# Performance work log

Measured on AMD Instinct MI355X. Metric: run time of the kernel, lower is better.

## Reference

```python
import jax, jax.numpy as jnp
import numpy as np

N = 50000
E_RAND = 800000
IN_CH = 128
HID = 128
HEADS = 8
HEAD_DIM = HID // HEADS  # 16
NUM_CLASSES = 40
NEG_SLOPE = 0.2


def _gatv2_conv(x, src, dst, Wl, Wr, att, b, concat):
    # Wl, Wr: [F_in, H*C]; att: [H, C]; b: [H*C] or [C]
    H, C = att.shape
    xl = (x @ Wl).reshape(N, H, C)  # source-side projection
    xr = (x @ Wr).reshape(N, H, C)  # target-side projection
    e = jax.nn.leaky_relu(xl[src] + xr[dst], NEG_SLOPE)      # [E,H,C]
    logits = jnp.einsum('ehc,hc->eh', e, att)                # [E,H]
    lmax = jax.ops.segment_max(logits, dst, num_segments=N)  # [N,H]
    lmax = jnp.where(jnp.isfinite(lmax), lmax, 0.0)
    p = jnp.exp(logits - lmax[dst])                          # [E,H]
    denom = jax.ops.segment_sum(p, dst, num_segments=N)      # [N,H]
    alpha = p / jnp.maximum(denom[dst], 1e-16)               # segment softmax
    out = jax.ops.segment_sum(xl[src] * alpha[:, :, None], dst, num_segments=N)  # [N,H,C]
    out = out.reshape(N, H * C) if concat else out.mean(axis=1)
    return out + b


def setup_inputs() -> dict:
    key = jax.random.key(0)
    ks = jax.random.split(key, 16)
    x = jax.random.normal(ks[0], (N, IN_CH), dtype=jnp.float32)
    src = jax.random.randint(ks[1], (E_RAND,), 0, N)
    dst = jax.random.randint(ks[2], (E_RAND,), 0, N)
    loops = jnp.arange(N)  # PyG GATv2Conv adds self-loops by default
    edge_src = jnp.concatenate([src, loops]).astype(jnp.int64)
    edge_dst = jnp.concatenate([dst, loops]).astype(jnp.int64)

    def glorot(k, shape):
        fan = shape[0] + shape[1]
        s = jnp.sqrt(6.0 / fan)
        return jax.random.uniform(k, shape, jnp.float32, -s, s)

    # layer 0: 128 -> 8 heads x 16, concat
    Wl0 = glorot(ks[3], (IN_CH, HID)); Wr0 = glorot(ks[4], (IN_CH, HID))
    att0 = glorot(ks[5], (HEADS, HEAD_DIM)); b0 = jnp.zeros((HID,), jnp.float32)
    # layer 1: 128 -> 8 heads x 16, concat
    Wl1 = glorot(ks[6], (HID, HID)); Wr1 = glorot(ks[7], (HID, HID))
    att1 = glorot(ks[8], (HEADS, HEAD_DIM)); b1 = jnp.zeros((HID,), jnp.float32)
    # layer 2: 128 -> 1 head x 40, no concat (mean == identity for 1 head)
    Wl2 = glorot(ks[9], (HID, NUM_CLASSES)); Wr2 = glorot(ks[10], (HID, NUM_CLASSES))
    att2 = glorot(ks[11], (1, NUM_CLASSES)); b2 = jnp.zeros((NUM_CLASSES,), jnp.float32)

    return {"x": x, "edge_src": edge_src, "edge_dst": edge_dst,
            "Wl0": Wl0, "Wr0": Wr0, "att0": att0, "b0": b0,
            "Wl1": Wl1, "Wr1": Wr1, "att1": att1, "b1": b1,
            "Wl2": Wl2, "Wr2": Wr2, "att2": att2, "b2": b2}


def reference(x, edge_src, edge_dst, Wl0, Wr0, att0, b0, Wl1, Wr1, att1, b1,
              Wl2, Wr2, att2, b2):
    # Inference mode: F.dropout(training=False) is identity.
    h = _gatv2_conv(x, edge_src, edge_dst, Wl0, Wr0, att0, b0, concat=True)
    h = jax.nn.relu(h)
    h = _gatv2_conv(h, edge_src, edge_dst, Wl1, Wr1, att1, b1, concat=True)
    h = jax.nn.relu(h)
    out = _gatv2_conv(h, edge_src, edge_dst, Wl2, Wr2, att2, b2, concat=False)
    return out
```

## Files before the change

kernel.cpp:

```cpp
#include <hip/hip_runtime.h>
#include <hip/hip_fp16.h>
#include <cmath>

typedef _Float16 half8 __attribute__((ext_vector_type(8)));
typedef _Float16 h2 __attribute__((ext_vector_type(2)));
typedef float f32x4 __attribute__((ext_vector_type(4)));

#define BINCAP 2600
#define BSTRIDE (BINCAP + 384)
#define NBINS_MAX 512

__global__ void fill_i32(int* __restrict__ p, int v, int n) {
    int i = blockIdx.x * blockDim.x + threadIdx.x;
    if (i < n) p[i] = v;
}

__device__ __forceinline__ float dpp_add_xor1(float t) {
    int r = __builtin_amdgcn_update_dpp(0, __float_as_int(t), 0xB1, 0xF, 0xF, true);
    return t + __int_as_float(r);
}
__device__ __forceinline__ float dpp_add_xor2(float t) {
    int r = __builtin_amdgcn_update_dpp(0, __float_as_int(t), 0x4E, 0xF, 0xF, true);
    return t + __int_as_float(r);
}

__device__ __forceinline__ float hdot2(h2 a, h2 b, float acc) {
#if __has_builtin(__builtin_amdgcn_fdot2)
    return __builtin_amdgcn_fdot2(a, b, acc, false);
#else
    return acc + (float)a[0] * (float)b[0] + (float)a[1] * (float)b[1];
#endif
}

__global__ __launch_bounds__(256) void bin_edges(const int* __restrict__ src,
                                                 const int* __restrict__ dst,
                                                 int* __restrict__ binCnt,
                                                 unsigned* __restrict__ binned,
                                                 int E, int nbins)
{
    __shared__ int hist[NBINS_MAX];
    __shared__ int ofs[NBINS_MAX];
    int tid = threadIdx.x;
    for (int i = tid; i < nbins; i += 256) hist[i] = 0;
    __syncthreads();
    int chunk = (E + gridDim.x - 1) / gridDim.x;
    int e0 = blockIdx.x * chunk;
    int e1 = min(e0 + chunk, E);
    for (int e = e0 + tid; e < e1; e += 256)
        atomicAdd(&hist[dst[e] >> 7], 1);
    __syncthreads();
    for (int b = tid; b < nbins; b += 256) {
        int h = hist[b];
        ofs[b] = (h > 0) ? atomicAdd(&binCnt[b], h) : 0;
    }
    __syncthreads();
    for (int e = e0 + tid; e < e1; e += 256) {
        int d = dst[e];
        int b = d >> 7;
        int p = atomicAdd(&ofs[b], 1);
        if (p < BINCAP)
            binned[(size_t)b * BINCAP + p] = (unsigned)src[e] | ((unsigned)(d & 127) << 16);
    }
}

__global__ __launch_bounds__(256) void bin_to_csr(const int* __restrict__ binCnt,
                                                  const unsigned* __restrict__ binned,
                                                  int* __restrict__ bucket,
                                                  int2* __restrict__ meta, int N)
{
    __shared__ int dcnt[128], ps[128], dpos[128];
    __shared__ int sbuf[BSTRIDE];
    __shared__ int tot_s;
    int b = blockIdx.x, tid = threadIdx.x;
    int nb = min(binCnt[b], BINCAP);
    size_t inbase = (size_t)b * BINCAP;
    size_t outbase = (size_t)b * BSTRIDE;
    if (tid < 128) dcnt[tid] = 0;
    __syncthreads();
    for (int i = tid; i < nb; i += 256)
        atomicAdd(&dcnt[(binned[inbase + i] >> 16) & 127], 1);
    __syncthreads();
    int pc = 0;
    if (tid < 128) { pc = (dcnt[tid] + 3) & ~3; ps[tid] = pc; }
    __syncthreads();
    for (int o = 1; o < 128; o <<= 1) {
        int v = (tid < 128 && tid >= o) ? ps[tid - o] : 0;
        __syncthreads();
        if (tid < 128) ps[tid] += v;
        __syncthreads();
    }
    if (tid < 128) {
        int dofs = ps[tid] - pc;
        dpos[tid] = dofs;
        for (int k = dcnt[tid]; k < pc; ++k) sbuf[dofs + k] = 0;
        int gd = b * 128 + tid;
        if (gd < N) meta[gd] = make_int2((int)outbase + dofs, dcnt[tid]);
        if (tid == 127) tot_s = ps[127];
    }
    __syncthreads();
    for (int i = tid; i < nb; i += 256) {
        unsigned u = binned[inbase + i];
        int p = atomicAdd(&dpos[(u >> 16) & 127], 1);
        sbuf[p] = (int)(u & 0xFFFFu);
    }
    __syncthreads();
    int tot = min(tot_s, BSTRIDE);
    for (int i = tid; i < tot; i += 256)
        bucket[outbase + i] = sbuf[i];
}

__global__ void wt_build(const float* __restrict__ Wl0, const float* __restrict__ Wr0,
                         const float* __restrict__ Wl1, const float* __restrict__ Wr1,
                         const float* __restrict__ Wl2, const float* __restrict__ Wr2,
                         __half* __restrict__ Wt0, __half* __restrict__ Wt1,
                         __half* __restrict__ Wt2) {
    int i = blockIdx.x * blockDim.x + threadIdx.x;
    const int T01 = 256 * 128, T2 = 80 * 128;
    if (i < T01) {
        int c = i >> 7, k = i & 127;
        float v = (c < 128) ? Wl0[k * 128 + c] : Wr0[k * 128 + (c - 128)];
        Wt0[i] = __float2half(v);
    } else if (i < 2 * T01) {
        int j = i - T01;
        int c = j >> 7, k = j & 127;
        float v = (c < 128) ? Wl1[k * 128 + c] : Wr1[k * 128 + (c - 128)];
        Wt1[j] = __float2half(v);
    } else if (i < 2 * T01 + T2) {
        int j = i - 2 * T01;
        int c = j >> 7, k = j & 127;
        float v = (c < 40) ? Wl2[k * 40 + c] : Wr2[k * 40 + (c - 40)];
        Wt2[j] = __float2half(v);
    }
}

template<int OUTH, bool HIN>
__global__ __launch_bounds__(256) void proj_mfma(const void* __restrict__ xin,
                                                 const __half* __restrict__ Wt,
                                                 __half* __restrict__ xl,
                                                 __half* __restrict__ xr,
                                                 int n)
{
    constexpr int OUTT = 2 * OUTH;
    constexpr int CT = OUTT / 16;
    __shared__ uint4 lds[1024 + OUTT * 16];
    int t = threadIdx.x;
    int r0 = blockIdx.x * 64;
    {
        int row = t >> 2;
        int k0 = (t & 3) * 32;
        int gr = r0 + row;
        #pragma unroll
        for (int s = 0; s < 4; ++s) {
            union { uint4 u; _Float16 h[8]; } pk;
            if (gr < n) {
                if constexpr (HIN) {
                    const uint4* xp = (const uint4*)((const __half*)xin + (size_t)gr * 128 + k0);
                    pk.u = xp[s];
                } else {
                    const float4* xp = (const float4*)((const float*)xin + (size_t)gr * 128 + k0 + s * 8);
                    float4 f0 = xp[0], f1 = xp[1];
                    pk.h[0] = (_Float16)f0.x; pk.h[1] = (_Float16)f0.y;
                    pk.h[2] = (_Float16)f0.z; pk.h[3] = (_Float16)f0.w;
                    pk.h[4] = (_Float16)f1.x; pk.h[5] = (_Float16)f1.y;
                    pk.h[6] = (_Float16)f1.z; pk.h[7] = (_Float16)f1.w;
                }
            } else {
                pk.u = make_uint4(0, 0, 0, 0);
            }
            int j = (t & 3) * 4 + s;
            lds[row * 16 + (j ^ (row & 7))] = pk.u;
        }
    }
    {
        const uint4* Wtv = (const uint4*)Wt;
        for (int m = t; m < OUTT * 16; m += 256) {
            int c = m >> 4, j = m & 15;
            lds[1024 + c * 16 + (j ^ (c & 7))] = Wtv[m];
        }
    }
    __syncthreads();
    int w = t >> 6, l = t & 63;
    int lr = l & 15, lg = l >> 4;
    half8 af[4];
    {
        int row = w * 16 + lr;
        #pragma unroll
        for (int kb = 0; kb < 4; ++kb) {
            int j = kb * 4 + lg;
            af[kb] = *reinterpret_cast<const half8*>(&lds[row * 16 + (j ^ (row & 7))]);
        }
    }
    f32x4 acc[CT];
    #pragma unroll
    for (int ct = 0; ct < CT; ++ct) acc[ct] = (f32x4){0.f, 0.f, 0.f, 0.f};
    int csw = lr & 7;
    #pragma unroll
    for (int ct = 0; ct < CT; ++ct) {
        int c = ct * 16 + lr;
        #pragma unroll
        for (int kb = 0; kb < 4; ++kb) {
            int j = kb * 4 + lg;
            half8 bf = *reinterpret_cast<const half8*>(&lds[1024 + c * 16 + (j ^ csw)]);
            acc[ct] = __builtin_amdgcn_mfma_f32_16x16x32_f16(af[kb], bf, acc[ct], 0, 0, 0);
        }
    }
    #pragma unroll
    for (int ct = 0; ct < CT; ++ct) {
        int c = ct * 16 + lr;
        #pragma unroll
        for (int i = 0; i < 4; ++i) {
            int gr = r0 + w * 16 + lg * 4 + i;
            if (gr < n) {
                __half h = __float2half(acc[ct][i]);
                if (c < OUTH) xl[(size_t)gr * OUTH + c] = h;
                else          xr[(size_t)gr * OUTH + (c - OUTH)] = h;
            }
        }
    }
}

__global__ void aggr128(const int2* __restrict__ meta, const int* __restrict__ bucket,
                        const __half* __restrict__ xlh, const __half* __restrict__ xrh,
                        const float* __restrict__ att, const float* __restrict__ bias,
                        __half* __restrict__ outp, int N, int do_relu)
{
    int wave = threadIdx.x >> 6;
    int lane = threadIdx.x & 63;
    int grp = lane >> 4;
    int j = lane & 15;
    int nd = (blockIdx.x * (blockDim.x >> 6) + wave) * 4 + grp;
    if (nd >= N) return;
    union { uint4 u; h2 h[4]; } rq;
    rq.u = ((const uint4*)xrh)[(size_t)nd * 16 + j];
    h2 a2[4];
    {
        float4 t0 = ((const float4*)att)[2 * j];
        float4 t1 = ((const float4*)att)[2 * j + 1];
        a2[0] = h2{(_Float16)t0.x, (_Float16)t0.y};
        a2[1] = h2{(_Float16)t0.z, (_Float16)t0.w};
        a2[2] = h2{(_Float16)t1.x, (_Float16)t1.y};
        a2[3] = h2{(_Float16)t1.z, (_Float16)t1.w};
    }
    const uint4* xlv = (const uint4*)xlh;
    int2 md = meta[nd];
    int beg = md.x, deg = md.y;
    const int* brow = bucket + beg;
    const h2 c02 = h2{(_Float16)0.2f, (_Float16)0.2f};
    float s0 = 0.f, s1 = 0.f, s2 = 0.f, s3 = 0.f;
    float o0[8], o1[8], o2[8], o3[8];
    #pragma unroll
    for (int i = 0; i < 8; ++i) { o0[i] = 0.f; o1[i] = 0.f; o2[i] = 0.f; o3[i] = 0.f; }
    for (int p = 0; p < deg; p += 4) {
        int4 ss = *(const int4*)(brow + p);
        union { uint4 u; h2 h[4]; } q0, q1, q2, q3;
        q0.u = xlv[(size_t)ss.x * 16 + j];
        q1.u = xlv[(size_t)ss.y * 16 + j];
        q2.u = xlv[(size_t)ss.z * 16 + j];
        q3.u = xlv[(size_t)ss.w * 16 + j];
        {
            float t = 0.f;
            #pragma unroll
            for (int i = 0; i < 4; ++i) {
                h2 v2 = q0.h[i] + rq.h[i];
                h2 lk = __builtin_elementwise_max(v2, v2 * c02);
                t = hdot2(lk, a2[i], t);
            }
            t = dpp_add_xor1(t);
            float pe = __expf(t);
            s0 += pe;
            #pragma unroll
            for (int i = 0; i < 4; ++i) {
                o0[2*i]   = fmaf(pe, (float)q0.h[i][0], o0[2*i]);
                o0[2*i+1] = fmaf(pe, (float)q0.h[i][1], o0[2*i+1]);
            }
        }
        {
            float t = 0.f;
            #pragma unroll
            for (int i = 0; i < 4; ++i) {
                h2 v2 = q1.h[i] + rq.h[i];
                h2 lk = __builtin_elementwise_max(v2, v2 * c02);
                t = hdot2(lk, a2[i], t);
            }
            t = dpp_add_xor1(t);
            float pe = (p + 1 < deg) ? __expf(t) : 0.f;
            s1 += pe;
            #pragma unroll
            for (int i = 0; i < 4; ++i) {
                o1[2*i]   = fmaf(pe, (float)q1.h[i][0], o1[2*i]);
                o1[2*i+1] = fmaf(pe, (float)q1.h[i][1], o1[2*i+1]);
            }
        }
        {
            float t = 0.f;
            #pragma unroll
            for (int i = 0; i < 4; ++i) {
                h2 v2 = q2.h[i] + rq.h[i];
                h2 lk = __builtin_elementwise_max(v2, v2 * c02);
                t = hdot2(lk, a2[i], t);
            }
            t = dpp_add_xor1(t);
            float pe = (p + 2 < deg) ? __expf(t) : 0.f;
            s2 += pe;
            #pragma unroll
            for (int i = 0; i < 4; ++i) {
                o2[2*i]   = fmaf(pe, (float)q2.h[i][0], o2[2*i]);
                o2[2*i+1] = fmaf(pe, (float)q2.h[i][1], o2[2*i+1]);
            }
        }
        {
            float t = 0.f;
            #pragma unroll
            for (int i = 0; i < 4; ++i) {
                h2 v2 = q3.h[i] + rq.h[i];
                h2 lk = __builtin_elementwise_max(v2, v2 * c02);
                t = hdot2(lk, a2[i], t);
            }
            t = dpp_add_xor1(t);
            float pe = (p + 3 < deg) ? __expf(t) : 0.f;
            s3 += pe;
            #pragma unroll
            for (int i = 0; i < 4; ++i) {
                o3[2*i]   = fmaf(pe, (float)q3.h[i][0], o3[2*i]);
                o3[2*i+1] = fmaf(pe, (float)q3.h[i][1], o3[2*i+1]);
            }
        }
    }
    float s = (s0 + s1) + (s2 + s3);
    {
        float inv = 1.f / fmaxf(s, 1e-16f);
        float4 b0 = ((const float4*)bias)[2 * j];
        float4 b1 = ((const float4*)bias)[2 * j + 1];
        float w[8];
        #pragma unroll
        for (int i = 0; i < 8; ++i)
            w[i] = ((o0[i] + o1[i]) + (o2[i] + o3[i])) * inv;
        w[0] += b0.x; w[1] += b0.y; w[2] += b0.z; w[3] += b0.w;
        w[4] += b1.x; w[5] += b1.y; w[6] += b1.z; w[7] += b1.w;
        if (do_relu) {
            #pragma unroll
            for (int i = 0; i < 8; ++i) w[i] = fmaxf(w[i], 0.f);
        }
        union { uint4 u; __half2 h[4]; } ow;
        ow.h[0] = __floats2half2_rn(w[0], w[1]);
        ow.h[1] = __floats2half2_rn(w[2], w[3]);
        ow.h[2] = __floats2half2_rn(w[4], w[5]);
        ow.h[3] = __floats2half2_rn(w[6], w[7]);
        ((uint4*)outp)[(size_t)nd * 16 + j] = ow.u;
    }
}

__global__ void aggr40(const int2* __restrict__ meta, const int* __restrict__ bucket,
                       const __half* __restrict__ xlh, const __half* __restrict__ xrh,
                       const float* __restrict__ att, const float* __restrict__ bias,
                       float* __restrict__ outp, int N)
{
    int wave = threadIdx.x >> 6;
    int lane = threadIdx.x & 63;
    int grp = lane >> 4;
    int j = lane & 15;
    int nd = (blockIdx.x * (blockDim.x >> 6) + wave) * 4 + grp;
    if (nd >= N) return;
    bool act = (j < 10);
    union { uint2 u; h2 h[2]; } rq;
    rq.u = make_uint2(0, 0);
    h2 a2[2] = {h2{(_Float16)0.f, (_Float16)0.f}, h2{(_Float16)0.f, (_Float16)0.f}};
    if (act) {
        rq.u = *(const uint2*)(xrh + (size_t)nd * 40 + 4 * j);
        float4 a4 = ((const float4*)att)[j];
        a2[0] = h2{(_Float16)a4.x, (_Float16)a4.y};
        a2[1] = h2{(_Float16)a4.z, (_Float16)a4.w};
    }
    int2 md = meta[nd];
    int beg = md.x, deg = md.y;
    const int* brow = bucket + beg;
    const h2 c02 = h2{(_Float16)0.2f, (_Float16)0.2f};
    float s0 = 0.f, s1 = 0.f;
    float o0[4], o1[4];
    #pragma unroll
    for (int i = 0; i < 4; ++i) { o0[i] = 0.f; o1[i] = 0.f; }
    for (int p = 0; p < deg; p += 4) {
        int4 ss = *(const int4*)(brow + p);
        union { uint2 u; h2 h[2]; } q0, q1, q2, q3;
        q0.u = act ? *(const uint2*)(xlh + (size_t)ss.x * 40 + 4 * j) : make_uint2(0, 0);
        q1.u = act ? *(const uint2*)(xlh + (size_t)ss.y * 40 + 4 * j) : make_uint2(0, 0);
        q2.u = act ? *(const uint2*)(xlh + (size_t)ss.z * 40 + 4 * j) : make_uint2(0, 0);
        q3.u = act ? *(const uint2*)(xlh + (size_t)ss.w * 40 + 4 * j) : make_uint2(0, 0);
        {
            float t = 0.f;
            #pragma unroll
            for (int i = 0; i < 2; ++i) {
                h2 v2 = q0.h[i] + rq.h[i];
                h2 lk = __builtin_elementwise_max(v2, v2 * c02);
                t = hdot2(lk, a2[i], t);
            }
            t = dpp_add_xor1(t); t = dpp_add_xor2(t);
            t += __shfl_xor(t, 4); t += __shfl_xor(t, 8);
            float pe = __expf(t);
            s0 += pe;
            #pragma unroll
            for (int i = 0; i < 2; ++i) {
                o0[2*i]   = fmaf(pe, (float)q0.h[i][0], o0[2*i]);
                o0[2*i+1] = fmaf(pe, (float)q0.h[i][1], o0[2*i+1]);
            }
        }
        {
            float t = 0.f;
            #pragma unroll
            for (int i = 0; i < 2; ++i) {
                h2 v2 = q1.h[i] + rq.h[i];
                h2 lk = __builtin_elementwise_max(v2, v2 * c02);
                t = hdot2(lk, a2[i], t);
            }
            t = dpp_add_xor1(t); t = dpp_add_xor2(t);
            t += __shfl_xor(t, 4); t += __shfl_xor(t, 8);
            float pe = (p + 1 < deg) ? __expf(t) : 0.f;
            s1 += pe;
            #pragma unroll
            for (int i = 0; i < 2; ++i) {
                o1[2*i]   = fmaf(pe, (float)q1.h[i][0], o1[2*i]);
                o1[2*i+1] = fmaf(pe, (float)q1.h[i][1], o1[2*i+1]);
            }
        }
        {
            float t = 0.f;
            #pragma unroll
            for (int i = 0; i < 2; ++i) {
                h2 v2 = q2.h[i] + rq.h[i];
                h2 lk = __builtin_elementwise_max(v2, v2 * c02);
                t = hdot2(lk, a2[i], t);
            }
            t = dpp_add_xor1(t); t = dpp_add_xor2(t);
            t += __shfl_xor(t, 4); t += __shfl_xor(t, 8);
            float pe = (p + 2 < deg) ? __expf(t) : 0.f;
            s0 += pe;
            #pragma unroll
            for (int i = 0; i < 2; ++i) {
                o0[2*i]   = fmaf(pe, (float)q2.h[i][0], o0[2*i]);
                o0[2*i+1] = fmaf(pe, (float)q2.h[i][1], o0[2*i+1]);
            }
        }
        {
            float t = 0.f;
            #pragma unroll
            for (int i = 0; i < 2; ++i) {
                h2 v2 = q3.h[i] + rq.h[i];
                h2 lk = __builtin_elementwise_max(v2, v2 * c02);
                t = hdot2(lk, a2[i], t);
            }
            t = dpp_add_xor1(t); t = dpp_add_xor2(t);
            t += __shfl_xor(t, 4); t += __shfl_xor(t, 8);
            float pe = (p + 3 < deg) ? __expf(t) : 0.f;
            s1 += pe;
            #pragma unroll
            for (int i = 0; i < 2; ++i) {
                o1[2*i]   = fmaf(pe, (float)q3.h[i][0], o1[2*i]);
                o1[2*i+1] = fmaf(pe, (float)q3.h[i][1], o1[2*i+1]);
            }
        }
    }
    if (act) {
        float s = s0 + s1;
        float inv = 1.f / fmaxf(s, 1e-16f);
        float4 b4 = ((const float4*)bias)[j];
        float4 w;
        w.x = (o0[0] + o1[0]) * inv + b4.x;
        w.y = (o0[1] + o1[1]) * inv + b4.y;
        w.z = (o0[2] + o1[2]) * inv + b4.z;
        w.w = (o0[3] + o1[3]) * inv + b4.w;
        *(float4*)(outp + (size_t)nd * 40 + 4 * j) = w;
    }
}

extern "C" void kernel_launch(void* const* d_in, const int* in_sizes, int n_in,
                              void* d_out, int out_size, void* d_ws, size_t ws_size,
                              hipStream_t stream)
{
    const float* x    = (const float*)d_in[0];
    const int*   esrc = (const int*)d_in[1];
    const int*   edst = (const int*)d_in[2];
    const float* Wl0  = (const float*)d_in[3];
    const float* Wr0  = (const float*)d_in[4];
    const float* att0 = (const float*)d_in[5];
    const float* b0   = (const float*)d_in[6];
    const float* Wl1  = (const float*)d_in[7];
    const float* Wr1  = (const float*)d_in[8];
    const float* att1 = (const float*)d_in[9];
    const float* b1   = (const float*)d_in[10];
    const float* Wl2  = (const float*)d_in[11];
    const float* Wr2  = (const float*)d_in[12];
    const float* att2 = (const float*)d_in[13];
    const float* b2   = (const float*)d_in[14];
    float* out = (float*)d_out;

    const int N = in_sizes[0] / 128;
    const int E = in_sizes[1];
    const int nbins = (N + 127) / 128;

    char* ws = (char*)d_ws;
    size_t off = 0;
    auto walloc = [&](size_t bytes) -> void* {
        void* p = ws + off;
        off = (off + bytes + 255) & ~(size_t)255;
        return p;
    };
    __half*   xlh    = (__half*)walloc((size_t)N * 128 * 2);
    __half*   xrh    = (__half*)walloc((size_t)N * 128 * 2);
    __half*   hbuf   = (__half*)walloc((size_t)N * 128 * 2);
    __half*   Wt0    = (__half*)walloc(256 * 128 * 2);
    __half*   Wt1    = (__half*)walloc(256 * 128 * 2);
    __half*   Wt2    = (__half*)walloc(80 * 128 * 2);
    int*      binCnt = (int*)walloc((size_t)nbins * 4);
    unsigned* binned = (unsigned*)walloc((size_t)nbins * BINCAP * 4);
    int*      bucket = (int*)walloc((size_t)nbins * BSTRIDE * 4);
    int2*     meta   = (int2*)walloc((size_t)N * 8);

    wt_build<<<(2 * 256 * 128 + 80 * 128 + 255) / 256, 256, 0, stream>>>(
        Wl0, Wr0, Wl1, Wr1, Wl2, Wr2, Wt0, Wt1, Wt2);

    fill_i32<<<(nbins + 255) / 256, 256, 0, stream>>>(binCnt, 0, nbins);
    bin_edges<<<256, 256, 0, stream>>>(esrc, edst, binCnt, binned, E, nbins);
    bin_to_csr<<<nbins, 256, 0, stream>>>(binCnt, binned, bucket, meta, N);

    int nblk = (N + 15) / 16;
    int pblk = (N + 63) / 64;

    proj_mfma<128, false><<<pblk, 256, 0, stream>>>(x, Wt0, xlh, xrh, N);
    aggr128<<<nblk, 256, 0, stream>>>(meta, bucket, xlh, xrh, att0, b0, hbuf, N, 1);
    proj_mfma<128, true><<<pblk, 256, 0, stream>>>(hbuf, Wt1, xlh, xrh, N);
    aggr128<<<nblk, 256, 0, stream>>>(meta, bucket, xlh, xrh, att1, b1, hbuf, N, 1);
    proj_mfma<40, true><<<pblk, 256, 0, stream>>>(hbuf, Wt2, xlh, xrh, N);
    aggr40<<<nblk, 256, 0, stream>>>(meta, bucket, xlh, xrh, att2, b2, out, N);
}
```

Baseline: 180.7 us.

## Sort destination nodes by degree and software-pipeline neighbor gathers in aggregation

Adds a degree histogram, scan and scatter that build a permutation of nodes grouped by in-degree, so each wave's four node groups get similar edge counts and idle less on divergent loop trip counts. The aggregation kernels also prefetch the next four neighbor rows while computing the current four, to hide gather latency. The fill kernel is replaced by hipMemsetAsync. This adds three small kernels plus extra live registers for the prefetch buffers, and output writes follow the permuted node order.

```diff
diff --git a/kernel.cpp b/kernel.cpp
--- a/kernel.cpp
+++ b/kernel.cpp
@@ -9,11 +9,6 @@
 #define BINCAP 2600
 #define BSTRIDE (BINCAP + 384)
 #define NBINS_MAX 512
-
-__global__ void fill_i32(int* __restrict__ p, int v, int n) {
-    int i = blockIdx.x * blockDim.x + threadIdx.x;
-    if (i < n) p[i] = v;
-}
 
 __device__ __forceinline__ float dpp_add_xor1(float t) {
     int r = __builtin_amdgcn_update_dpp(0, __float_as_int(t), 0xB1, 0xF, 0xF, true);
@@ -107,6 +102,44 @@
     int tot = min(tot_s, BSTRIDE);
     for (int i = tid; i < tot; i += 256)
         bucket[outbase + i] = sbuf[i];
+}
+
+__global__ void deg_hist(const int2* __restrict__ meta, int* __restrict__ hist, int N) {
+    __shared__ int lh[256];
+    int tid = threadIdx.x;
+    lh[tid] = 0;
+    __syncthreads();
+    int i = blockIdx.x * blockDim.x + tid;
+    int stride = gridDim.x * blockDim.x;
+    for (; i < N; i += stride)
+        atomicAdd(&lh[min(meta[i].y, 255)], 1);
+    __syncthreads();
+    if (lh[tid] > 0) atomicAdd(&hist[tid], lh[tid]);
+}
+
+__global__ void scan_hist(const int* __restrict__ hist, int* __restrict__ dofs) {
+    __shared__ int b[256];
+    int t = threadIdx.x;
+    int v = hist[t];
+    b[t] = v;
+    __syncthreads();
+    for (int o = 1; o < 256; o <<= 1) {
+        int x = (t >= o) ? b[t - o] : 0;
+        __syncthreads();
+        b[t] += x;
+        __syncthreads();
+    }
+    dofs[t] = b[t] - v;
+}
+
+__global__ void perm_scatter(const int2* __restrict__ meta, int* __restrict__ dofs,
+                             int* __restrict__ perm, int N) {
+    int i = blockIdx.x * blockDim.x + threadIdx.x;
+    int stride = gridDim.x * blockDim.x;
+    for (; i < N; i += stride) {
+        int pos = atomicAdd(&dofs[min(meta[i].y, 255)], 1);
+        perm[pos] = i;
+    }
 }
 
 __global__ void wt_build(const float* __restrict__ Wl0, const float* __restrict__ Wr0,
@@ -219,7 +252,8 @@
     }
 }
 
-__global__ void aggr128(const int2* __restrict__ meta, const int* __restrict__ bucket,
+__global__ void aggr128(const int* __restrict__ perm,
+                        const int2* __restrict__ meta, const int* __restrict__ bucket,
                         const __half* __restrict__ xlh, const __half* __restrict__ xrh,
                         const float* __restrict__ att, const float* __restrict__ bias,
                         __half* __restrict__ outp, int N, int do_relu)
@@ -228,8 +262,9 @@
     int lane = threadIdx.x & 63;
     int grp = lane >> 4;
     int j = lane & 15;
-    int nd = (blockIdx.x * (blockDim.x >> 6) + wave) * 4 + grp;
-    if (nd >= N) return;
+    int ndv = (blockIdx.x * (blockDim.x >> 6) + wave) * 4 + grp;
+    if (ndv >= N) return;
+    int nd = perm[ndv];
     union { uint4 u; h2 h[4]; } rq;
     rq.u = ((const uint4*)xrh)[(size_t)nd * 16 + j];
     h2 a2[4];
@@ -250,18 +285,31 @@
     float o0[8], o1[8], o2[8], o3[8];
     #pragma unroll
     for (int i = 0; i < 8; ++i) { o0[i] = 0.f; o1[i] = 0.f; o2[i] = 0.f; o3[i] = 0.f; }
+    uint4 qa0, qa1, qa2, qa3;
+    {
+        int4 ss = *(const int4*)(brow);
+        qa0 = xlv[(size_t)ss.x * 16 + j];
+        qa1 = xlv[(size_t)ss.y * 16 + j];
+        qa2 = xlv[(size_t)ss.z * 16 + j];
+        qa3 = xlv[(size_t)ss.w * 16 + j];
+    }
     for (int p = 0; p < deg; p += 4) {
-        int4 ss = *(const int4*)(brow + p);
-        union { uint4 u; h2 h[4]; } q0, q1, q2, q3;
-        q0.u = xlv[(size_t)ss.x * 16 + j];
-        q1.u = xlv[(size_t)ss.y * 16 + j];
-        q2.u = xlv[(size_t)ss.z * 16 + j];
-        q3.u = xlv[(size_t)ss.w * 16 + j];
-        {
-            float t = 0.f;
-            #pragma unroll
-            for (int i = 0; i < 4; ++i) {
-                h2 v2 = q0.h[i] + rq.h[i];
+        uint4 qb0, qb1, qb2, qb3;
+        {
+            int pn = (p + 4 < deg) ? p + 4 : p;
+            int4 sn = *(const int4*)(brow + pn);
+            qb0 = xlv[(size_t)sn.x * 16 + j];
+            qb1 = xlv[(size_t)sn.y * 16 + j];
+            qb2 = xlv[(size_t)sn.z * 16 + j];
+            qb3 = xlv[(size_t)sn.w * 16 + j];
+        }
+        union { uint4 u; h2 h[4]; } q;
+        {
+            q.u = qa0;
+            float t = 0.f;
+            #pragma unroll
+            for (int i = 0; i < 4; ++i) {
+                h2 v2 = q.h[i] + rq.h[i];
                 h2 lk = __builtin_elementwise_max(v2, v2 * c02);
                 t = hdot2(lk, a2[i], t);
             }
@@ -270,15 +318,16 @@
             s0 += pe;
             #pragma unroll
             for (int i = 0; i < 4; ++i) {
-                o0[2*i]   = fmaf(pe, (float)q0.h[i][0], o0[2*i]);
-                o0[2*i+1] = fmaf(pe, (float)q0.h[i][1], o0[2*i+1]);
-            }
-        }
-        {
-            float t = 0.f;
-            #pragma unroll
-            for (int i = 0; i < 4; ++i) {
-                h2 v2 = q1.h[i] + rq.h[i];
+                o0[2*i]   = fmaf(pe, (float)q.h[i][0], o0[2*i]);
+                o0[2*i+1] = fmaf(pe, (float)q.h[i][1], o0[2*i+1]);
+            }
+        }
+        {
+            q.u = qa1;
+            float t = 0.f;
+            #pragma unroll
+            for (int i = 0; i < 4; ++i) {
+                h2 v2 = q.h[i] + rq.h[i];
                 h2 lk = __builtin_elementwise_max(v2, v2 * c02);
                 t = hdot2(lk, a2[i], t);
             }
@@ -287,15 +336,16 @@
             s1 += pe;
             #pragma unroll
             for (int i = 0; i < 4; ++i) {
-                o1[2*i]   = fmaf(pe, (float)q1.h[i][0], o1[2*i]);
-                o1[2*i+1] = fmaf(pe, (float)q1.h[i][1], o1[2*i+1]);
-            }
-        }
-        {
-            float t = 0.f;
-            #pragma unroll
-            for (int i = 0; i < 4; ++i) {
-                h2 v2 = q2.h[i] + rq.h[i];
+                o1[2*i]   = fmaf(pe, (float)q.h[i][0], o1[2*i]);
+                o1[2*i+1] = fmaf(pe, (float)q.h[i][1], o1[2*i+1]);
+            }
+        }
+        {
+            q.u = qa2;
+            float t = 0.f;
+            #pragma unroll
+            for (int i = 0; i < 4; ++i) {
+                h2 v2 = q.h[i] + rq.h[i];
                 h2 lk = __builtin_elementwise_max(v2, v2 * c02);
                 t = hdot2(lk, a2[i], t);
             }
@@ -304,15 +354,16 @@
             s2 += pe;
             #pragma unroll
             for (int i = 0; i < 4; ++i) {
-                o2[2*i]   = fmaf(pe, (float)q2.h[i][0], o2[2*i]);
-                o2[2*i+1] = fmaf(pe, (float)q2.h[i][1], o2[2*i+1]);
-            }
-        }
-        {
-            float t = 0.f;
-            #pragma unroll
-            for (int i = 0; i < 4; ++i) {
-                h2 v2 = q3.h[i] + rq.h[i];
+                o2[2*i]   = fmaf(pe, (float)q.h[i][0], o2[2*i]);
+                o2[2*i+1] = fmaf(pe, (float)q.h[i][1], o2[2*i+1]);
+            }
+        }
+        {
+            q.u = qa3;
+            float t = 0.f;
+            #pragma unroll
+            for (int i = 0; i < 4; ++i) {
+                h2 v2 = q.h[i] + rq.h[i];
                 h2 lk = __builtin_elementwise_max(v2, v2 * c02);
                 t = hdot2(lk, a2[i], t);
             }
@@ -321,10 +372,11 @@
             s3 += pe;
             #pragma unroll
             for (int i = 0; i < 4; ++i) {
-                o3[2*i]   = fmaf(pe, (float)q3.h[i][0], o3[2*i]);
-                o3[2*i+1] = fmaf(pe, (float)q3.h[i][1], o3[2*i+1]);
-            }
-        }
+                o3[2*i]   = fmaf(pe, (float)q.h[i][0], o3[2*i]);
+                o3[2*i+1] = fmaf(pe, (float)q.h[i][1], o3[2*i+1]);
+            }
+        }
+        qa0 = qb0; qa1 = qb1; qa2 = qb2; qa3 = qb3;
     }
     float s = (s0 + s1) + (s2 + s3);
     {
@@ -350,7 +402,8 @@
     }
 }
 
-__global__ void aggr40(const int2* __restrict__ meta, const int* __restrict__ bucket,
+__global__ void aggr40(const int* __restrict__ perm,
+                       const int2* __restrict__ meta, const int* __restrict__ bucket,
                        const __half* __restrict__ xlh, const __half* __restrict__ xrh,
                        const float* __restrict__ att, const float* __restrict__ bias,
                        float* __restrict__ outp, int N)
@@ -359,8 +412,9 @@
     int lane = threadIdx.x & 63;
     int grp = lane >> 4;
     int j = lane & 15;
-    int nd = (blockIdx.x * (blockDim.x >> 6) + wave) * 4 + grp;
-    if (nd >= N) return;
+    int ndv = (blockIdx.x * (blockDim.x >> 6) + wave) * 4 + grp;
+    if (ndv >= N) return;
+    int nd = perm[ndv];
     bool act = (j < 10);
     union { uint2 u; h2 h[2]; } rq;
     rq.u = make_uint2(0, 0);
@@ -379,18 +433,31 @@
     float o0[4], o1[4];
     #pragma unroll
     for (int i = 0; i < 4; ++i) { o0[i] = 0.f; o1[i] = 0.f; }
+    uint2 qa0, qa1, qa2, qa3;
+    {
+        int4 ss = *(const int4*)(brow);
+        qa0 = act ? *(const uint2*)(xlh + (size_t)ss.x * 40 + 4 * j) : make_uint2(0, 0);
+        qa1 = act ? *(const uint2*)(xlh + (size_t)ss.y * 40 + 4 * j) : make_uint2(0, 0);
+        qa2 = act ? *(const uint2*)(xlh + (size_t)ss.z * 40 + 4 * j) : make_uint2(0, 0);
+        qa3 = act ? *(const uint2*)(xlh + (size_t)ss.w * 40 + 4 * j) : make_uint2(0, 0);
+    }
     for (int p = 0; p < deg; p += 4) {
-        int4 ss = *(const int4*)(brow + p);
-        union { uint2 u; h2 h[2]; } q0, q1, q2, q3;
-        q0.u = act ? *(const uint2*)(xlh + (size_t)ss.x * 40 + 4 * j) : make_uint2(0, 0);
-        q1.u = act ? *(const uint2*)(xlh + (size_t)ss.y * 40 + 4 * j) : make_uint2(0, 0);
-        q2.u = act ? *(const uint2*)(xlh + (size_t)ss.z * 40 + 4 * j) : make_uint2(0, 0);
-        q3.u = act ? *(const uint2*)(xlh + (size_t)ss.w * 40 + 4 * j) : make_uint2(0, 0);
-        {
-            float t = 0.f;
-            #pragma unroll
-            for (int i = 0; i < 2; ++i) {
-                h2 v2 = q0.h[i] + rq.h[i];
+        uint2 qb0, qb1, qb2, qb3;
+        {
+            int pn = (p + 4 < deg) ? p + 4 : p;
+            int4 sn = *(const int4*)(brow + pn);
+            qb0 = act ? *(const uint2*)(xlh + (size_t)sn.x * 40 + 4 * j) : make_uint2(0, 0);
+            qb1 = act ? *(const uint2*)(xlh + (size_t)sn.y * 40 + 4 * j) : make_uint2(0, 0);
+            qb2 = act ? *(const uint2*)(xlh + (size_t)sn.z * 40 + 4 * j) : make_uint2(0, 0);
+            qb3 = act ? *(const uint2*)(xlh + (size_t)sn.w * 40 + 4 * j) : make_uint2(0, 0);
+        }
+        union { uint2 u; h2 h[2]; } q;
+        {
+            q.u = qa0;
+            float t = 0.f;
+            #pragma unroll
+            for (int i = 0; i < 2; ++i) {
+                h2 v2 = q.h[i] + rq.h[i];
                 h2 lk = __builtin_elementwise_max(v2, v2 * c02);
                 t = hdot2(lk, a2[i], t);
             }
@@ -400,15 +467,16 @@
             s0 += pe;
             #pragma unroll
             for (int i = 0; i < 2; ++i) {
-                o0[2*i]   = fmaf(pe, (float)q0.h[i][0], o0[2*i]);
-                o0[2*i+1] = fmaf(pe, (float)q0.h[i][1], o0[2*i+1]);
-            }
-        }
-        {
-            float t = 0.f;
-            #pragma unroll
-            for (int i = 0; i < 2; ++i) {
-                h2 v2 = q1.h[i] + rq.h[i];
+                o0[2*i]   = fmaf(pe, (float)q.h[i][0], o0[2*i]);
+                o0[2*i+1] = fmaf(pe, (float)q.h[i][1], o0[2*i+1]);
+            }
+        }
+        {
+            q.u = qa1;
+            float t = 0.f;
+            #pragma unroll
+            for (int i = 0; i < 2; ++i) {
+                h2 v2 = q.h[i] + rq.h[i];
                 h2 lk = __builtin_elementwise_max(v2, v2 * c02);
                 t = hdot2(lk, a2[i], t);
             }
@@ -418,15 +486,16 @@
             s1 += pe;
             #pragma unroll
             for (int i = 0; i < 2; ++i) {
-                o1[2*i]   = fmaf(pe, (float)q1.h[i][0], o1[2*i]);
-                o1[2*i+1] = fmaf(pe, (float)q1.h[i][1], o1[2*i+1]);
-            }
-        }
-        {
-            float t = 0.f;
-            #pragma unroll
-            for (int i = 0; i < 2; ++i) {
-                h2 v2 = q2.h[i] + rq.h[i];
+                o1[2*i]   = fmaf(pe, (float)q.h[i][0], o1[2*i]);
+                o1[2*i+1] = fmaf(pe, (float)q.h[i][1], o1[2*i+1]);
+            }
+        }
+        {
+            q.u = qa2;
+            float t = 0.f;
+            #pragma unroll
+            for (int i = 0; i < 2; ++i) {
+                h2 v2 = q.h[i] + rq.h[i];
                 h2 lk = __builtin_elementwise_max(v2, v2 * c02);
                 t = hdot2(lk, a2[i], t);
             }
@@ -436,15 +505,16 @@
             s0 += pe;
             #pragma unroll
             for (int i = 0; i < 2; ++i) {
-                o0[2*i]   = fmaf(pe, (float)q2.h[i][0], o0[2*i]);
-                o0[2*i+1] = fmaf(pe, (float)q2.h[i][1], o0[2*i+1]);
-            }
-        }
-        {
-            float t = 0.f;
-            #pragma unroll
-            for (int i = 0; i < 2; ++i) {
-                h2 v2 = q3.h[i] + rq.h[i];
+                o0[2*i]   = fmaf(pe, (float)q.h[i][0], o0[2*i]);
+                o0[2*i+1] = fmaf(pe, (float)q.h[i][1], o0[2*i+1]);
+            }
+        }
+        {
+            q.u = qa3;
+            float t = 0.f;
+            #pragma unroll
+            for (int i = 0; i < 2; ++i) {
+                h2 v2 = q.h[i] + rq.h[i];
                 h2 lk = __builtin_elementwise_max(v2, v2 * c02);
                 t = hdot2(lk, a2[i], t);
             }
@@ -454,10 +524,11 @@
             s1 += pe;
             #pragma unroll
             for (int i = 0; i < 2; ++i) {
-                o1[2*i]   = fmaf(pe, (float)q3.h[i][0], o1[2*i]);
-                o1[2*i+1] = fmaf(pe, (float)q3.h[i][1], o1[2*i+1]);
-            }
-        }
+                o1[2*i]   = fmaf(pe, (float)q.h[i][0], o1[2*i]);
+                o1[2*i+1] = fmaf(pe, (float)q.h[i][1], o1[2*i+1]);
+            }
+        }
+        qa0 = qb0; qa1 = qb1; qa2 = qb2; qa3 = qb3;
     }
     if (act) {
         float s = s0 + s1;
@@ -514,21 +585,29 @@
     unsigned* binned = (unsigned*)walloc((size_t)nbins * BINCAP * 4);
     int*      bucket = (int*)walloc((size_t)nbins * BSTRIDE * 4);
     int2*     meta   = (int2*)walloc((size_t)N * 8);
+    int*      hist   = (int*)walloc(256 * 4);
+    int*      dofs   = (int*)walloc(256 * 4);
+    int*      perm   = (int*)walloc((size_t)N * 4);
 
     wt_build<<<(2 * 256 * 128 + 80 * 128 + 255) / 256, 256, 0, stream>>>(
         Wl0, Wr0, Wl1, Wr1, Wl2, Wr2, Wt0, Wt1, Wt2);
 
-    fill_i32<<<(nbins + 255) / 256, 256, 0, stream>>>(binCnt, 0, nbins);
+    hipMemsetAsync(binCnt, 0, (size_t)nbins * 4, stream);
+    hipMemsetAsync(hist, 0, 256 * 4, stream);
     bin_edges<<<256, 256, 0, stream>>>(esrc, edst, binCnt, binned, E, nbins);
     bin_to_csr<<<nbins, 256, 0, stream>>>(binCnt, binned, bucket, meta, N);
 
+    deg_hist<<<256, 256, 0, stream>>>(meta, hist, N);
+    scan_hist<<<1, 256, 0, stream>>>(hist, dofs);
+    perm_scatter<<<256, 256, 0, stream>>>(meta, dofs, perm, N);
+
     int nblk = (N + 15) / 16;
     int pblk = (N + 63) / 64;
 
     proj_mfma<128, false><<<pblk, 256, 0, stream>>>(x, Wt0, xlh, xrh, N);
-    aggr128<<<nblk, 256, 0, stream>>>(meta, bucket, xlh, xrh, att0, b0, hbuf, N, 1);
+    aggr128<<<nblk, 256, 0, stream>>>(perm, meta, bucket, xlh, xrh, att0, b0, hbuf, N, 1);
     proj_mfma<128, true><<<pblk, 256, 0, stream>>>(hbuf, Wt1, xlh, xrh, N);
-    aggr128<<<nblk, 256, 0, stream>>>(meta, bucket, xlh, xrh, att1, b1, hbuf, N, 1);
+    aggr128<<<nblk, 256, 0, stream>>>(perm, meta, bucket, xlh, xrh, att1, b1, hbuf, N, 1);
     proj_mfma<40, true><<<pblk, 256, 0, stream>>>(hbuf, Wt2, xlh, xrh, N);
-    aggr40<<<nblk, 256, 0, stream>>>(meta, bucket, xlh, xrh, att2, b2, out, N);
-}
+    aggr40<<<nblk, 256, 0, stream>>>(perm, meta, bucket, xlh, xrh, att2, b2, out, N);
+}
```

After: 331.3 us. 83.4% more time.
